# Kernel optimization log

Hardware: AMD Instinct MI355X
Metric: run time of the kernel (lower is better)

Reference implementation:

```python
import jax, jax.numpy as jnp
import numpy as np

B, S, HID, QK, H = 2, 2048, 2048, 2048, 16
DK, DV = QK // H, HID // H
EPS = 1e-5


def setup_inputs() -> dict:
    key = jax.random.key(0)
    ks = jax.random.split(key, 8)
    sd = 1.0 / np.sqrt(HID)
    inp = {
        "x": jax.random.normal(ks[0], (B, S, HID), jnp.float32),
        "wq": jax.random.normal(ks[1], (HID, QK), jnp.float32) * sd,
        "bq": jnp.zeros((QK,), jnp.float32),
        "wk": jax.random.normal(ks[2], (HID, QK), jnp.float32) * sd,
        "bk": jnp.zeros((QK,), jnp.float32),
        "wv": jax.random.normal(ks[3], (HID, HID), jnp.float32) * sd,
        "bv": jnp.zeros((HID,), jnp.float32),
        "wg": jax.random.normal(ks[4], (HID, HID), jnp.float32) * sd,
        "bg": jnp.zeros((HID,), jnp.float32),
        "wo": jax.random.normal(ks[5], (HID, HID), jnp.float32) * sd,
        "bo": jnp.zeros((HID,), jnp.float32),
        "gn_w": jnp.ones((HID,), jnp.float32),
        "gn_b": jnp.zeros((HID,), jnp.float32),
        # RetNet default gammas: 1 - exp(linspace(log(1/32), log(1/512), H))
        "gamma": 1.0 - jnp.exp(jnp.linspace(-np.log(32.0), -np.log(512.0), H)).astype(jnp.float32),
    }
    return inp


def reference(x, wq, bq, wk, bk, wv, bv, wg, bg, wo, bo, gn_w, gn_b, gamma):
    b, s, hid = x.shape
    h = gamma.shape[0]
    dk = wq.shape[1] // h
    dv = hid // h
    # projections + head split -> (b, h, s, d)
    q = (x @ wq + bq).reshape(b, s, h, dk).transpose(0, 2, 1, 3)
    k = (x @ wk + bk).reshape(b, s, h, dk).transpose(0, 2, 1, 3)
    v = (x @ wv + bv).reshape(b, s, h, dv).transpose(0, 2, 1, 3)
    # causal decay mask: gamma^(n-m) for n >= m else 0  -> (h, s, s)
    idx = jnp.arange(s)
    diff = idx[:, None] - idx[None, :]
    expn = jnp.maximum(diff, 0).astype(x.dtype)
    dmask = jnp.where(diff >= 0, gamma[:, None, None] ** expn, 0.0)
    # parallel retention
    scores = jnp.einsum('bhnd,bhmd->bhnm', q, k) * dmask
    ret = jnp.einsum('bhnm,bhmv->bhnv', scores, v)  # (b, h, s, dv)
    # GroupNorm(num_groups=h) over (b, hid, s): stats per (b, head) over (s, dv)
    mean = ret.mean(axis=(2, 3), keepdims=True)
    var = ((ret - mean) ** 2).mean(axis=(2, 3), keepdims=True)
    norm = (ret - mean) * jax.lax.rsqrt(var + EPS)
    norm = norm * gn_w.reshape(h, dv)[None, :, None, :] + gn_b.reshape(h, dv)[None, :, None, :]
    ro = norm.transpose(0, 2, 1, 3).reshape(b, s, hid)  # (b, s, hid)
    gate = jax.nn.silu(x @ wg + bg)
    out = (gate * ro) @ wo + bo
    return out
```

## Files before the change

kernel.cpp:

```cpp
#include <hip/hip_runtime.h>
#include <cstdint>
#include <cstddef>

#define DEVI __device__ __forceinline__

typedef unsigned short u16;
typedef __bf16 bf16_t;
typedef bf16_t bf16x8 __attribute__((ext_vector_type(8)));
typedef float f32x4 __attribute__((ext_vector_type(4)));

constexpr int BB = 2, SS = 2048, HID = 2048, NH = 16, DK = 128, DV = 128;
constexpr int MR = BB * SS;
constexpr int KD = HID;

DEVI u16 f2bf(float f) {
  union { float f; uint32_t u; } v; v.f = f;
  uint32_t u = v.u;
  uint32_t r = u + 0x7FFFu + ((u >> 16) & 1u);
  return (u16)(r >> 16);
}
DEVI float bf2f(u16 h) {
  union { uint32_t u; float f; } v; v.u = ((uint32_t)h) << 16;
  return v.f;
}
DEVI f32x4 mfma16(bf16x8 a, bf16x8 b, f32x4 c) {
  return __builtin_amdgcn_mfma_f32_16x16x32_bf16(a, b, c, 0, 0, 0);
}
DEVI void gload16(const u16* g, u16* l) {
  __builtin_amdgcn_global_load_lds(
      (const __attribute__((address_space(1))) uint32_t*)g,
      (__attribute__((address_space(3))) uint32_t*)l, 16, 0, 0);
}

__global__ __launch_bounds__(256) void castx_kernel(
    const float* __restrict__ x, u16* __restrict__ xb)
{
  size_t i = ((size_t)blockIdx.x * 256 + threadIdx.x) * 8;
  float4 a = *(const float4*)(x + i);
  float4 b = *(const float4*)(x + i + 4);
  ushort4 lo, hi;
  lo.x = f2bf(a.x); lo.y = f2bf(a.y); lo.z = f2bf(a.z); lo.w = f2bf(a.w);
  hi.x = f2bf(b.x); hi.y = f2bf(b.y); hi.z = f2bf(b.z); hi.w = f2bf(b.w);
  *(ushort4*)(xb + i) = lo;
  *(ushort4*)(xb + i + 4) = hi;
}

__global__ __launch_bounds__(256) void wtrans_kernel(
    const float* __restrict__ wq, const float* __restrict__ wk,
    const float* __restrict__ wv, const float* __restrict__ wg,
    const float* __restrict__ wo, u16* __restrict__ wt)
{
  __shared__ float t[32][33];
  const float* srcs[5] = {wq, wk, wv, wg, wo};
  const float* W = srcs[blockIdx.z];
  u16* dst = wt + (size_t)blockIdx.z * (size_t)KD * HID;
  int tx = threadIdx.x, ty = threadIdx.y;
  int c0 = blockIdx.x * 32, r0 = blockIdx.y * 32;
#pragma unroll
  for (int i = 0; i < 4; ++i)
    t[ty + i * 8][tx] = W[(size_t)(r0 + ty + i * 8) * HID + c0 + tx];
  __syncthreads();
#pragma unroll
  for (int i = 0; i < 4; ++i) {
    int n = c0 + ty + i * 8;
    int k = r0 + tx;
    dst[(size_t)n * KD + k] = f2bf(t[tx][ty + i * 8]);
  }
}

DEVI void gemm_core(const u16* __restrict__ A, const u16* __restrict__ Bt,
                    int m0, int n0, u16* sA, u16* sB, f32x4 (&acc)[4][4])
{
  const int tid = threadIdx.x;
  const int lane = tid & 63;
  const int wave = tid >> 6;
  const int wr = wave >> 1, wc = wave & 1;
  const int lhi = lane >> 4, llo = lane & 15;

  for (int kt = 0; kt < KD / 64; ++kt) {
    __syncthreads();
#pragma unroll
    for (int i = 0; i < 4; ++i) {
      int c = i * 256 + wave * 64 + lane;
      int row = c >> 3, scol = c & 7;
      int dcol = scol ^ (row & 7);
      gload16(A + (size_t)(m0 + row) * KD + kt * 64 + dcol * 8,
              sA + (i * 256 + wave * 64) * 8);
    }
#pragma unroll
    for (int i = 0; i < 4; ++i) {
      int c = i * 256 + wave * 64 + lane;
      int row = c >> 3, scol = c & 7;
      int dcol = scol ^ (row & 7);
      gload16(Bt + (size_t)(n0 + row) * KD + kt * 64 + dcol * 8,
              sB + (i * 256 + wave * 64) * 8);
    }
    __syncthreads();
#pragma unroll
    for (int ks = 0; ks < 2; ++ks) {
      const int kb = ks * 64 + lhi * 16;
      bf16x8 af[4], bfr[4];
#pragma unroll
      for (int mi = 0; mi < 4; ++mi) {
        int row = wr * 64 + mi * 16 + llo;
        af[mi] = *(const bf16x8*)((char*)sA + row * 128 + (kb ^ ((row & 7) << 4)));
      }
#pragma unroll
      for (int ni = 0; ni < 4; ++ni) {
        int row = wc * 64 + ni * 16 + llo;
        bfr[ni] = *(const bf16x8*)((char*)sB + row * 128 + (kb ^ ((row & 7) << 4)));
      }
#pragma unroll
      for (int mi = 0; mi < 4; ++mi)
#pragma unroll
        for (int ni = 0; ni < 4; ++ni)
          acc[mi][ni] = mfma16(af[mi], bfr[ni], acc[mi][ni]);
    }
  }
}

__global__ __launch_bounds__(256) void proj_kernel(
    const u16* __restrict__ xb, const u16* __restrict__ wtBase,
    const float* __restrict__ bq, const float* __restrict__ bk,
    const float* __restrict__ bv, const float* __restrict__ bg,
    u16* __restrict__ qb, u16* __restrict__ kb,
    u16* __restrict__ vtb, u16* __restrict__ gb)
{
  __shared__ u16 sA[128 * 64];
  __shared__ u16 sB[128 * 64];
  const int z = blockIdx.z;
  const u16* Bt = wtBase + (size_t)z * (size_t)KD * HID;
  f32x4 acc[4][4];
  const f32x4 zero = {0.f, 0.f, 0.f, 0.f};
#pragma unroll
  for (int mi = 0; mi < 4; ++mi)
#pragma unroll
    for (int ni = 0; ni < 4; ++ni) acc[mi][ni] = zero;

  const int m0 = blockIdx.x * 128, n0 = blockIdx.y * 128;
  gemm_core(xb, Bt, m0, n0, sA, sB, acc);

  const float* bias = (z == 0) ? bq : (z == 1) ? bk : (z == 2) ? bv : bg;
  const int lane = threadIdx.x & 63, wave = threadIdx.x >> 6;
  const int wr = wave >> 1, wc = wave & 1;
  const int lhi = lane >> 4, llo = lane & 15;
#pragma unroll
  for (int mi = 0; mi < 4; ++mi) {
#pragma unroll
    for (int ni = 0; ni < 4; ++ni) {
      int row0 = m0 + wr * 64 + mi * 16 + lhi * 4;
      int n = n0 + wc * 64 + ni * 16 + llo;
      float bsn = bias[n];
      if (z == 2) {
        int b = row0 >> 11, s0 = row0 & (SS - 1);
        int h = n >> 7, j = n & 127;
        ushort4 hv;
        hv.x = f2bf(acc[mi][ni][0] + bsn);
        hv.y = f2bf(acc[mi][ni][1] + bsn);
        hv.z = f2bf(acc[mi][ni][2] + bsn);
        hv.w = f2bf(acc[mi][ni][3] + bsn);
        *(ushort4*)(vtb + ((size_t)((b * NH + h) * DV + j)) * SS + s0) = hv;
      } else if (z == 3) {
#pragma unroll
        for (int r = 0; r < 4; ++r) {
          int m = row0 + r;
          float c = acc[mi][ni][r] + bsn;
          float sg = c / (1.0f + expf(-c));
          gb[(size_t)m * HID + n] = f2bf(sg);
        }
      } else {
        u16* dst = (z == 0) ? qb : kb;
#pragma unroll
        for (int r = 0; r < 4; ++r) {
          int m = row0 + r;
          int b = m >> 11, s = m & (SS - 1);
          int h = n >> 7, j = n & 127;
          dst[((size_t)((b * NH + h) * SS + s)) * DK + j] = f2bf(acc[mi][ni][r] + bsn);
        }
      }
    }
  }
}

__global__ __launch_bounds__(256) void retention_kernel(
    const u16* __restrict__ qb, const u16* __restrict__ kb,
    const u16* __restrict__ vtb, const float* __restrict__ gamma,
    float* __restrict__ ret, float* __restrict__ stats)
{
  __shared__ u16 sK[64 * 128];
  __shared__ u16 sV[128 * 64];
  __shared__ u16 sP[4][32 * 64];
  __shared__ float red[8];

  const int bh = blockIdx.y;
  const int n0 = blockIdx.x * 128;
  const int h = bh & (NH - 1);
  const float lg2 = log2f(gamma[h]);

  const int tid = threadIdx.x, lane = tid & 63, wave = tid >> 6;
  const int lhi = lane >> 4, llo = lane & 15;
  const int qrow = n0 + wave * 32;

  const u16* qbase = qb + ((size_t)bh * SS + qrow) * DK;
  bf16x8 aq[2][4];
#pragma unroll
  for (int mi = 0; mi < 2; ++mi)
#pragma unroll
    for (int ks = 0; ks < 4; ++ks)
      aq[mi][ks] = *(const bf16x8*)(qbase + (size_t)(mi * 16 + llo) * DK + ks * 32 + lhi * 8);

  float rdec[2][4];
#pragma unroll
  for (int mi = 0; mi < 2; ++mi)
#pragma unroll
    for (int r = 0; r < 4; ++r)
      rdec[mi][r] = exp2f(lg2 * (float)(qrow + mi * 16 + lhi * 4 + r));

  const f32x4 zero = {0.f, 0.f, 0.f, 0.f};
  f32x4 oacc[2][8];
#pragma unroll
  for (int mi = 0; mi < 2; ++mi)
#pragma unroll
    for (int nj = 0; nj < 8; ++nj) oacc[mi][nj] = zero;

  const u16* kbase = kb + (size_t)bh * SS * DK;
  const u16* vbase = vtb + (size_t)bh * DV * SS;
  const int mtiles = n0 / 64 + 2;

  for (int mt = 0; mt < mtiles; ++mt) {
    const int m0 = mt * 64;
    __syncthreads();
#pragma unroll
    for (int i = 0; i < 4; ++i) {
      int c = i * 256 + wave * 64 + lane;
      int row = c >> 4, scol = c & 15;
      int dcol = scol ^ (row & 15);
      gload16(kbase + (size_t)(m0 + row) * DK + dcol * 8,
              sK + (i * 256 + wave * 64) * 8);
    }
#pragma unroll
    for (int i = 0; i < 4; ++i) {
      int c = i * 256 + wave * 64 + lane;
      int row = c >> 3, scol = c & 7;
      int dcol = scol ^ (row & 7);
      gload16(vbase + (size_t)row * SS + m0 + dcol * 8,
              sV + (i * 256 + wave * 64) * 8);
    }
    __syncthreads();

    f32x4 sacc[2][4];
#pragma unroll
    for (int mi = 0; mi < 2; ++mi)
#pragma unroll
      for (int ni = 0; ni < 4; ++ni) sacc[mi][ni] = zero;
#pragma unroll
    for (int ks = 0; ks < 4; ++ks) {
      const int kbyte = ks * 64 + lhi * 16;
      bf16x8 bk_[4];
#pragma unroll
      for (int ni = 0; ni < 4; ++ni) {
        int row = ni * 16 + llo;
        bk_[ni] = *(const bf16x8*)((char*)sK + row * 256 + (kbyte ^ ((row & 15) << 4)));
      }
#pragma unroll
      for (int mi = 0; mi < 2; ++mi)
#pragma unroll
        for (int ni = 0; ni < 4; ++ni)
          sacc[mi][ni] = mfma16(aq[mi][ks], bk_[ni], sacc[mi][ni]);
    }

    float cfac[4];
#pragma unroll
    for (int ni = 0; ni < 4; ++ni)
      cfac[ni] = exp2f(-lg2 * (float)(m0 + ni * 16 + llo));
    const bool masked = (m0 + 63 > qrow);
    char* myP = (char*)&sP[wave][0];
#pragma unroll
    for (int mi = 0; mi < 2; ++mi) {
#pragma unroll
      for (int ni = 0; ni < 4; ++ni) {
#pragma unroll
        for (int r = 0; r < 4; ++r) {
          int prow = mi * 16 + lhi * 4 + r;
          int pcol = ni * 16 + llo;
          float w = rdec[mi][r] * cfac[ni];
          if (masked && (qrow + prow < m0 + pcol)) w = 0.0f;
          float p = sacc[mi][ni][r] * w;
          *(u16*)(myP + prow * 128 + ((pcol * 2) ^ ((prow & 7) << 4))) = f2bf(p);
        }
      }
    }

#pragma unroll
    for (int ks2 = 0; ks2 < 2; ++ks2) {
      const int kbyte = ks2 * 64 + lhi * 16;
      bf16x8 pa[2];
#pragma unroll
      for (int mi = 0; mi < 2; ++mi) {
        int row = mi * 16 + llo;
        pa[mi] = *(const bf16x8*)(myP + row * 128 + (kbyte ^ ((row & 7) << 4)));
      }
#pragma unroll
      for (int nj = 0; nj < 8; ++nj) {
        int row = nj * 16 + llo;
        bf16x8 vb = *(const bf16x8*)((char*)sV + row * 128 + (kbyte ^ ((row & 7) << 4)));
#pragma unroll
        for (int mi = 0; mi < 2; ++mi)
          oacc[mi][nj] = mfma16(pa[mi], vb, oacc[mi][nj]);
      }
    }
  }

  float lsum = 0.f, lsq = 0.f;
  float* rbase = ret + ((size_t)bh * SS + qrow) * DV;
#pragma unroll
  for (int mi = 0; mi < 2; ++mi) {
#pragma unroll
    for (int nj = 0; nj < 8; ++nj) {
      int prow0 = mi * 16 + lhi * 4;
      int j = nj * 16 + llo;
#pragma unroll
      for (int r = 0; r < 4; ++r) {
        float v = oacc[mi][nj][r];
        rbase[(size_t)(prow0 + r) * DV + j] = v;
        lsum += v; lsq += v * v;
      }
    }
  }
#pragma unroll
  for (int off = 32; off > 0; off >>= 1) {
    lsum += __shfl_down(lsum, off, 64);
    lsq  += __shfl_down(lsq,  off, 64);
  }
  if (lane == 0) { red[wave * 2] = lsum; red[wave * 2 + 1] = lsq; }
  __syncthreads();
  if (tid == 0) {
    float s = red[0] + red[2] + red[4] + red[6];
    float q = red[1] + red[3] + red[5] + red[7];
    atomicAdd(&stats[bh * 2], s);
    atomicAdd(&stats[bh * 2 + 1], q);
  }
}

__global__ __launch_bounds__(256) void normgate_kernel(
    const float* __restrict__ ret, const u16* __restrict__ gb,
    const float* __restrict__ stats, const float* __restrict__ gn_w,
    const float* __restrict__ gn_b, u16* __restrict__ a2)
{
  const int idx4 = (blockIdx.x * 256 + threadIdx.x) * 4;
  const int bh = idx4 >> 18;
  const int rem = idx4 & (SS * DV - 1);
  const int s = rem >> 7;
  const int dv = rem & (DV - 1);
  const float inv = 1.0f / (float)(SS * DV);
  float mean = stats[bh * 2] * inv;
  float var = stats[bh * 2 + 1] * inv - mean * mean;
  float rstd = rsqrtf(var + 1e-5f);
  const int b = bh >> 4, h = bh & (NH - 1);
  const int hd = h * DV + dv;
  float4 rv = *(const float4*)(ret + idx4);
  float4 w4 = *(const float4*)(gn_w + hd);
  float4 b4 = *(const float4*)(gn_b + hd);
  size_t gidx = ((size_t)(b * SS + s)) * HID + hd;
  ushort4 g4 = *(const ushort4*)(gb + gidx);
  ushort4 o;
  o.x = f2bf(bf2f(g4.x) * ((rv.x - mean) * rstd * w4.x + b4.x));
  o.y = f2bf(bf2f(g4.y) * ((rv.y - mean) * rstd * w4.y + b4.y));
  o.z = f2bf(bf2f(g4.z) * ((rv.z - mean) * rstd * w4.z + b4.z));
  o.w = f2bf(bf2f(g4.w) * ((rv.w - mean) * rstd * w4.w + b4.w));
  *(ushort4*)(a2 + gidx) = o;
}

__global__ __launch_bounds__(256) void final_kernel(
    const u16* __restrict__ a2, const u16* __restrict__ woT,
    const float* __restrict__ bo, float* __restrict__ out)
{
  __shared__ u16 sA[128 * 64];
  __shared__ u16 sB[128 * 64];
  f32x4 acc[4][4];
  const f32x4 zero = {0.f, 0.f, 0.f, 0.f};
#pragma unroll
  for (int mi = 0; mi < 4; ++mi)
#pragma unroll
    for (int ni = 0; ni < 4; ++ni) acc[mi][ni] = zero;

  const int m0 = blockIdx.x * 128, n0 = blockIdx.y * 128;
  gemm_core(a2, woT, m0, n0, sA, sB, acc);

  const int lane = threadIdx.x & 63, wave = threadIdx.x >> 6;
  const int wr = wave >> 1, wc = wave & 1;
  const int lhi = lane >> 4, llo = lane & 15;
#pragma unroll
  for (int mi = 0; mi < 4; ++mi) {
#pragma unroll
    for (int ni = 0; ni < 4; ++ni) {
      int row0 = m0 + wr * 64 + mi * 16 + lhi * 4;
      int n = n0 + wc * 64 + ni * 16 + llo;
      float bn = bo[n];
#pragma unroll
      for (int r = 0; r < 4; ++r)
        out[(size_t)(row0 + r) * HID + n] = acc[mi][ni][r] + bn;
    }
  }
}

extern "C" void kernel_launch(void* const* d_in, const int* in_sizes, int n_in,
                              void* d_out, int out_size, void* d_ws, size_t ws_size,
                              hipStream_t stream) {
  const float* x    = (const float*)d_in[0];
  const float* wq   = (const float*)d_in[1];
  const float* bq   = (const float*)d_in[2];
  const float* wk   = (const float*)d_in[3];
  const float* bk   = (const float*)d_in[4];
  const float* wv   = (const float*)d_in[5];
  const float* bv   = (const float*)d_in[6];
  const float* wg   = (const float*)d_in[7];
  const float* bg   = (const float*)d_in[8];
  const float* wo   = (const float*)d_in[9];
  const float* bo   = (const float*)d_in[10];
  const float* gn_w = (const float*)d_in[11];
  const float* gn_b = (const float*)d_in[12];
  const float* gam  = (const float*)d_in[13];

  char* ws = (char*)d_ws;
  u16* wT    = (u16*)(ws);
  u16* qb    = (u16*)(ws + 41943040);
  u16* kbuf  = (u16*)(ws + 58720256);
  u16* vtb   = (u16*)(ws + 75497472);
  u16* gb    = (u16*)(ws + 92274688);
  float* ret = (float*)(ws + 109051904);
  float* st  = (float*)(ws + 142606336);
  u16* a2    = qb;
  u16* xb    = (u16*)ret;

  hipMemsetAsync(st, 0, 256, stream);
  castx_kernel<<<4096, 256, 0, stream>>>(x, xb);
  wtrans_kernel<<<dim3(64, 64, 5), dim3(32, 8), 0, stream>>>(wq, wk, wv, wg, wo, wT);
  proj_kernel<<<dim3(32, 16, 4), 256, 0, stream>>>(xb, wT, bq, bk, bv, bg, qb, kbuf, vtb, gb);
  retention_kernel<<<dim3(16, 32), 256, 0, stream>>>(qb, kbuf, vtb, gam, ret, st);
  normgate_kernel<<<16384, 256, 0, stream>>>(ret, gb, st, gn_w, gn_b, a2);
  final_kernel<<<dim3(32, 16), 256, 0, stream>>>(a2, wT + (size_t)4 * KD * HID, bo, (float*)d_out);
}
```

Baseline: 555.7 us.

## Double-buffer GEMM and retention tiles, enlarge GEMM tiles, stage epilogue through LDS

The projection and output GEMMs move from 128x128 to 256x256 tiles with 512 threads and double-buffered LDS, so the load of the next K slice overlaps the MFMA work on the current one. The retention kernel also double-buffers its K/V tiles and raises wave priority around its MFMA sections. GEMM epilogues now go through swizzled LDS so global stores are coalesced 16-byte writes. Costs: 128KB of LDS per block and fewer blocks (128 for the final GEMM), which lowers occupancy and can leave CUs underused.

```diff
diff --git a/kernel.cpp b/kernel.cpp
--- a/kernel.cpp
+++ b/kernel.cpp
@@ -10,7 +10,6 @@
 typedef float f32x4 __attribute__((ext_vector_type(4)));
 
 constexpr int BB = 2, SS = 2048, HID = 2048, NH = 16, DK = 128, DV = 128;
-constexpr int MR = BB * SS;
 constexpr int KD = HID;
 
 DEVI u16 f2bf(float f) {
@@ -68,90 +67,100 @@
   }
 }
 
-DEVI void gemm_core(const u16* __restrict__ A, const u16* __restrict__ Bt,
-                    int m0, int n0, u16* sA, u16* sB, f32x4 (&acc)[4][4])
-{
-  const int tid = threadIdx.x;
-  const int lane = tid & 63;
-  const int wave = tid >> 6;
-  const int wr = wave >> 1, wc = wave & 1;
+DEVI void stage256(const u16* __restrict__ A, const u16* __restrict__ Bt,
+                   int m0, int n0, int kt, u16* sa, u16* sb, int tid)
+{
+#pragma unroll
+  for (int i = 0; i < 4; ++i) {
+    int c = i * 512 + tid;
+    int row = c >> 3, scol = c & 7, dcol = scol ^ (row & 7);
+    gload16(A + (size_t)(m0 + row) * KD + kt * 64 + dcol * 8, sa + c * 8);
+  }
+#pragma unroll
+  for (int i = 0; i < 4; ++i) {
+    int c = i * 512 + tid;
+    int row = c >> 3, scol = c & 7, dcol = scol ^ (row & 7);
+    gload16(Bt + (size_t)(n0 + row) * KD + kt * 64 + dcol * 8, sb + c * 8);
+  }
+}
+
+DEVI void gemm256(const u16* __restrict__ A, const u16* __restrict__ Bt,
+                  int m0, int n0, char* smem, f32x4 (&acc)[8][4])
+{
+  const int tid = threadIdx.x, lane = tid & 63, wave = tid >> 6;
+  const int wr = wave >> 2, wc = wave & 3;
   const int lhi = lane >> 4, llo = lane & 15;
 
+  stage256(A, Bt, m0, n0, 0, (u16*)smem, (u16*)(smem + 65536), tid);
+  asm volatile("s_waitcnt vmcnt(0)" ::: "memory");
+  __syncthreads();
+
   for (int kt = 0; kt < KD / 64; ++kt) {
-    __syncthreads();
-#pragma unroll
-    for (int i = 0; i < 4; ++i) {
-      int c = i * 256 + wave * 64 + lane;
-      int row = c >> 3, scol = c & 7;
-      int dcol = scol ^ (row & 7);
-      gload16(A + (size_t)(m0 + row) * KD + kt * 64 + dcol * 8,
-              sA + (i * 256 + wave * 64) * 8);
-    }
-#pragma unroll
-    for (int i = 0; i < 4; ++i) {
-      int c = i * 256 + wave * 64 + lane;
-      int row = c >> 3, scol = c & 7;
-      int dcol = scol ^ (row & 7);
-      gload16(Bt + (size_t)(n0 + row) * KD + kt * 64 + dcol * 8,
-              sB + (i * 256 + wave * 64) * 8);
-    }
-    __syncthreads();
+    char* cA = smem + (kt & 1) * 32768;
+    char* cB = smem + 65536 + (kt & 1) * 32768;
+    if (kt + 1 < KD / 64) {
+      u16* nA = (u16*)(smem + ((kt + 1) & 1) * 32768);
+      u16* nB = (u16*)(smem + 65536 + ((kt + 1) & 1) * 32768);
+      stage256(A, Bt, m0, n0, kt + 1, nA, nB, tid);
+    }
+    __builtin_amdgcn_s_setprio(1);
 #pragma unroll
     for (int ks = 0; ks < 2; ++ks) {
       const int kb = ks * 64 + lhi * 16;
-      bf16x8 af[4], bfr[4];
-#pragma unroll
-      for (int mi = 0; mi < 4; ++mi) {
-        int row = wr * 64 + mi * 16 + llo;
-        af[mi] = *(const bf16x8*)((char*)sA + row * 128 + (kb ^ ((row & 7) << 4)));
-      }
+      bf16x8 bfr[4];
 #pragma unroll
       for (int ni = 0; ni < 4; ++ni) {
         int row = wc * 64 + ni * 16 + llo;
-        bfr[ni] = *(const bf16x8*)((char*)sB + row * 128 + (kb ^ ((row & 7) << 4)));
-      }
-#pragma unroll
-      for (int mi = 0; mi < 4; ++mi)
+        bfr[ni] = *(const bf16x8*)(cB + row * 128 + (kb ^ ((row & 7) << 4)));
+      }
+#pragma unroll
+      for (int mi = 0; mi < 8; ++mi) {
+        int row = wr * 128 + mi * 16 + llo;
+        bf16x8 af = *(const bf16x8*)(cA + row * 128 + (kb ^ ((row & 7) << 4)));
 #pragma unroll
         for (int ni = 0; ni < 4; ++ni)
-          acc[mi][ni] = mfma16(af[mi], bfr[ni], acc[mi][ni]);
-    }
-  }
-}
-
-__global__ __launch_bounds__(256) void proj_kernel(
+          acc[mi][ni] = mfma16(af, bfr[ni], acc[mi][ni]);
+      }
+    }
+    __builtin_amdgcn_s_setprio(0);
+    asm volatile("s_waitcnt vmcnt(0)" ::: "memory");
+    __syncthreads();
+  }
+}
+
+__global__ __launch_bounds__(512, 2) void proj_kernel(
     const u16* __restrict__ xb, const u16* __restrict__ wtBase,
     const float* __restrict__ bq, const float* __restrict__ bk,
     const float* __restrict__ bv, const float* __restrict__ bg,
     u16* __restrict__ qb, u16* __restrict__ kb,
     u16* __restrict__ vtb, u16* __restrict__ gb)
 {
-  __shared__ u16 sA[128 * 64];
-  __shared__ u16 sB[128 * 64];
+  __shared__ __align__(16) char smem[131072];
   const int z = blockIdx.z;
   const u16* Bt = wtBase + (size_t)z * (size_t)KD * HID;
-  f32x4 acc[4][4];
+  f32x4 acc[8][4];
   const f32x4 zero = {0.f, 0.f, 0.f, 0.f};
 #pragma unroll
-  for (int mi = 0; mi < 4; ++mi)
+  for (int mi = 0; mi < 8; ++mi)
 #pragma unroll
     for (int ni = 0; ni < 4; ++ni) acc[mi][ni] = zero;
 
-  const int m0 = blockIdx.x * 128, n0 = blockIdx.y * 128;
-  gemm_core(xb, Bt, m0, n0, sA, sB, acc);
-
+  const int m0 = blockIdx.x * 256, n0 = blockIdx.y * 256;
+  gemm256(xb, Bt, m0, n0, smem, acc);
+
+  const int tid = threadIdx.x, lane = tid & 63, wave = tid >> 6;
+  const int wr = wave >> 2, wc = wave & 3;
+  const int lhi = lane >> 4, llo = lane & 15;
   const float* bias = (z == 0) ? bq : (z == 1) ? bk : (z == 2) ? bv : bg;
-  const int lane = threadIdx.x & 63, wave = threadIdx.x >> 6;
-  const int wr = wave >> 1, wc = wave & 1;
-  const int lhi = lane >> 4, llo = lane & 15;
-#pragma unroll
-  for (int mi = 0; mi < 4; ++mi) {
-#pragma unroll
-    for (int ni = 0; ni < 4; ++ni) {
-      int row0 = m0 + wr * 64 + mi * 16 + lhi * 4;
-      int n = n0 + wc * 64 + ni * 16 + llo;
-      float bsn = bias[n];
-      if (z == 2) {
+
+  if (z == 2) {
+#pragma unroll
+    for (int mi = 0; mi < 8; ++mi) {
+#pragma unroll
+      for (int ni = 0; ni < 4; ++ni) {
+        int row0 = m0 + wr * 128 + mi * 16 + lhi * 4;
+        int n = n0 + wc * 64 + ni * 16 + llo;
+        float bsn = bias[n];
         int b = row0 >> 11, s0 = row0 & (SS - 1);
         int h = n >> 7, j = n & 127;
         ushort4 hv;
@@ -160,23 +169,40 @@
         hv.z = f2bf(acc[mi][ni][2] + bsn);
         hv.w = f2bf(acc[mi][ni][3] + bsn);
         *(ushort4*)(vtb + ((size_t)((b * NH + h) * DV + j)) * SS + s0) = hv;
-      } else if (z == 3) {
+      }
+    }
+  } else {
+    u16* Lb = (u16*)smem;
+#pragma unroll
+    for (int mi = 0; mi < 8; ++mi) {
+#pragma unroll
+      for (int ni = 0; ni < 4; ++ni) {
+        int colL = wc * 64 + ni * 16 + llo;
+        float bsn = bias[n0 + colL];
 #pragma unroll
         for (int r = 0; r < 4; ++r) {
-          int m = row0 + r;
+          int rowL = wr * 128 + mi * 16 + lhi * 4 + r;
           float c = acc[mi][ni][r] + bsn;
-          float sg = c / (1.0f + expf(-c));
-          gb[(size_t)m * HID + n] = f2bf(sg);
+          if (z == 3) c = c / (1.0f + expf(-c));
+          Lb[rowL * 256 + (colL ^ (((rowL >> 2) & 3) << 4))] = f2bf(c);
         }
+      }
+    }
+    __syncthreads();
+    int rr = tid & 255, chh = tid >> 8;
+    int m = m0 + rr, b = m >> 11, s = m & (SS - 1);
+    int swz = ((rr >> 2) & 3) << 4;
+#pragma unroll
+    for (int jj = 0; jj < 16; ++jj) {
+      int c0 = chh * 128 + jj * 8;
+      uint4 v = *(const uint4*)&Lb[rr * 256 + (c0 ^ swz)];
+      int n = n0 + c0;
+      if (z == 3) {
+        *(uint4*)(gb + (size_t)m * HID + n) = v;
       } else {
+        int h = n >> 7, j2 = n & 127;
         u16* dst = (z == 0) ? qb : kb;
-#pragma unroll
-        for (int r = 0; r < 4; ++r) {
-          int m = row0 + r;
-          int b = m >> 11, s = m & (SS - 1);
-          int h = n >> 7, j = n & 127;
-          dst[((size_t)((b * NH + h) * SS + s)) * DK + j] = f2bf(acc[mi][ni][r] + bsn);
-        }
+        *(uint4*)(dst + ((size_t)((b * NH + h) * SS + s)) * DK + j2) = v;
       }
     }
   }
@@ -187,9 +213,7 @@
     const u16* __restrict__ vtb, const float* __restrict__ gamma,
     float* __restrict__ ret, float* __restrict__ stats)
 {
-  __shared__ u16 sK[64 * 128];
-  __shared__ u16 sV[128 * 64];
-  __shared__ u16 sP[4][32 * 64];
+  __shared__ __align__(16) char smemR[81920];
   __shared__ float red[8];
 
   const int bh = blockIdx.y;
@@ -227,32 +251,39 @@
   const u16* vbase = vtb + (size_t)bh * DV * SS;
   const int mtiles = n0 / 64 + 2;
 
+  auto stageKV = [&](int mbase, u16* sk, u16* sv) {
+#pragma unroll
+    for (int i = 0; i < 4; ++i) {
+      int c = i * 256 + tid;
+      int row = c >> 4, scol = c & 15, dcol = scol ^ (row & 15);
+      gload16(kbase + (size_t)(mbase + row) * DK + dcol * 8, sk + c * 8);
+    }
+#pragma unroll
+    for (int i = 0; i < 4; ++i) {
+      int c = i * 256 + tid;
+      int row = c >> 3, scol = c & 7, dcol = scol ^ (row & 7);
+      gload16(vbase + (size_t)row * SS + mbase + dcol * 8, sv + c * 8);
+    }
+  };
+
+  stageKV(0, (u16*)smemR, (u16*)(smemR + 32768));
+  asm volatile("s_waitcnt vmcnt(0)" ::: "memory");
+  __syncthreads();
+
   for (int mt = 0; mt < mtiles; ++mt) {
     const int m0 = mt * 64;
-    __syncthreads();
-#pragma unroll
-    for (int i = 0; i < 4; ++i) {
-      int c = i * 256 + wave * 64 + lane;
-      int row = c >> 4, scol = c & 15;
-      int dcol = scol ^ (row & 15);
-      gload16(kbase + (size_t)(m0 + row) * DK + dcol * 8,
-              sK + (i * 256 + wave * 64) * 8);
-    }
-#pragma unroll
-    for (int i = 0; i < 4; ++i) {
-      int c = i * 256 + wave * 64 + lane;
-      int row = c >> 3, scol = c & 7;
-      int dcol = scol ^ (row & 7);
-      gload16(vbase + (size_t)row * SS + m0 + dcol * 8,
-              sV + (i * 256 + wave * 64) * 8);
-    }
-    __syncthreads();
+    char* cK = smemR + (mt & 1) * 16384;
+    char* cV = smemR + 32768 + (mt & 1) * 16384;
+    if (mt + 1 < mtiles)
+      stageKV(m0 + 64, (u16*)(smemR + ((mt + 1) & 1) * 16384),
+              (u16*)(smemR + 32768 + ((mt + 1) & 1) * 16384));
 
     f32x4 sacc[2][4];
 #pragma unroll
     for (int mi = 0; mi < 2; ++mi)
 #pragma unroll
       for (int ni = 0; ni < 4; ++ni) sacc[mi][ni] = zero;
+    __builtin_amdgcn_s_setprio(1);
 #pragma unroll
     for (int ks = 0; ks < 4; ++ks) {
       const int kbyte = ks * 64 + lhi * 16;
@@ -260,7 +291,7 @@
 #pragma unroll
       for (int ni = 0; ni < 4; ++ni) {
         int row = ni * 16 + llo;
-        bk_[ni] = *(const bf16x8*)((char*)sK + row * 256 + (kbyte ^ ((row & 15) << 4)));
+        bk_[ni] = *(const bf16x8*)(cK + row * 256 + (kbyte ^ ((row & 15) << 4)));
       }
 #pragma unroll
       for (int mi = 0; mi < 2; ++mi)
@@ -268,13 +299,14 @@
         for (int ni = 0; ni < 4; ++ni)
           sacc[mi][ni] = mfma16(aq[mi][ks], bk_[ni], sacc[mi][ni]);
     }
+    __builtin_amdgcn_s_setprio(0);
 
     float cfac[4];
 #pragma unroll
     for (int ni = 0; ni < 4; ++ni)
       cfac[ni] = exp2f(-lg2 * (float)(m0 + ni * 16 + llo));
     const bool masked = (m0 + 63 > qrow);
-    char* myP = (char*)&sP[wave][0];
+    char* myP = smemR + 65536 + wave * 4096;
 #pragma unroll
     for (int mi = 0; mi < 2; ++mi) {
 #pragma unroll
@@ -291,6 +323,7 @@
       }
     }
 
+    __builtin_amdgcn_s_setprio(1);
 #pragma unroll
     for (int ks2 = 0; ks2 < 2; ++ks2) {
       const int kbyte = ks2 * 64 + lhi * 16;
@@ -303,12 +336,15 @@
 #pragma unroll
       for (int nj = 0; nj < 8; ++nj) {
         int row = nj * 16 + llo;
-        bf16x8 vb = *(const bf16x8*)((char*)sV + row * 128 + (kbyte ^ ((row & 7) << 4)));
+        bf16x8 vb = *(const bf16x8*)(cV + row * 128 + (kbyte ^ ((row & 7) << 4)));
 #pragma unroll
         for (int mi = 0; mi < 2; ++mi)
           oacc[mi][nj] = mfma16(pa[mi], vb, oacc[mi][nj]);
       }
     }
+    __builtin_amdgcn_s_setprio(0);
+    asm volatile("s_waitcnt vmcnt(0)" ::: "memory");
+    __syncthreads();
   }
 
   float lsum = 0.f, lsq = 0.f;
@@ -371,36 +407,55 @@
   *(ushort4*)(a2 + gidx) = o;
 }
 
-__global__ __launch_bounds__(256) void final_kernel(
+__global__ __launch_bounds__(512, 2) void final_kernel(
     const u16* __restrict__ a2, const u16* __restrict__ woT,
     const float* __restrict__ bo, float* __restrict__ out)
 {
-  __shared__ u16 sA[128 * 64];
-  __shared__ u16 sB[128 * 64];
-  f32x4 acc[4][4];
+  __shared__ __align__(16) char smem[131072];
+  f32x4 acc[8][4];
   const f32x4 zero = {0.f, 0.f, 0.f, 0.f};
 #pragma unroll
-  for (int mi = 0; mi < 4; ++mi)
+  for (int mi = 0; mi < 8; ++mi)
 #pragma unroll
     for (int ni = 0; ni < 4; ++ni) acc[mi][ni] = zero;
 
-  const int m0 = blockIdx.x * 128, n0 = blockIdx.y * 128;
-  gemm_core(a2, woT, m0, n0, sA, sB, acc);
-
-  const int lane = threadIdx.x & 63, wave = threadIdx.x >> 6;
-  const int wr = wave >> 1, wc = wave & 1;
+  const int m0 = blockIdx.x * 256, n0 = blockIdx.y * 256;
+  gemm256(a2, woT, m0, n0, smem, acc);
+
+  const int tid = threadIdx.x, lane = tid & 63, wave = tid >> 6;
+  const int wr = wave >> 2, wc = wave & 3;
   const int lhi = lane >> 4, llo = lane & 15;
-#pragma unroll
-  for (int mi = 0; mi < 4; ++mi) {
-#pragma unroll
-    for (int ni = 0; ni < 4; ++ni) {
-      int row0 = m0 + wr * 64 + mi * 16 + lhi * 4;
-      int n = n0 + wc * 64 + ni * 16 + llo;
-      float bn = bo[n];
-#pragma unroll
-      for (int r = 0; r < 4; ++r)
-        out[(size_t)(row0 + r) * HID + n] = acc[mi][ni][r] + bn;
-    }
+  float* Lf = (float*)smem;
+
+#pragma unroll
+  for (int pass = 0; pass < 2; ++pass) {
+    if ((wc >> 1) == pass) {
+#pragma unroll
+      for (int mi = 0; mi < 8; ++mi) {
+#pragma unroll
+        for (int ni = 0; ni < 4; ++ni) {
+          int colL = (wc & 1) * 64 + ni * 16 + llo;
+          float bn = bo[n0 + pass * 128 + colL];
+#pragma unroll
+          for (int r = 0; r < 4; ++r) {
+            int rowL = wr * 128 + mi * 16 + lhi * 4 + r;
+            Lf[rowL * 128 + (colL ^ (((rowL >> 2) & 1) << 4))] =
+                acc[mi][ni][r] + bn;
+          }
+        }
+      }
+    }
+    __syncthreads();
+    int rr = tid & 255, chh = tid >> 8;
+    int m = m0 + rr;
+    int swz = ((rr >> 2) & 1) << 4;
+#pragma unroll
+    for (int jj = 0; jj < 16; ++jj) {
+      int c0 = chh * 64 + jj * 4;
+      float4 v = *(const float4*)&Lf[rr * 128 + (c0 ^ swz)];
+      *(float4*)(out + (size_t)m * HID + n0 + pass * 128 + c0) = v;
+    }
+    __syncthreads();
   }
 }
 
@@ -436,8 +491,8 @@
   hipMemsetAsync(st, 0, 256, stream);
   castx_kernel<<<4096, 256, 0, stream>>>(x, xb);
   wtrans_kernel<<<dim3(64, 64, 5), dim3(32, 8), 0, stream>>>(wq, wk, wv, wg, wo, wT);
-  proj_kernel<<<dim3(32, 16, 4), 256, 0, stream>>>(xb, wT, bq, bk, bv, bg, qb, kbuf, vtb, gb);
+  proj_kernel<<<dim3(16, 8, 4), 512, 0, stream>>>(xb, wT, bq, bk, bv, bg, qb, kbuf, vtb, gb);
   retention_kernel<<<dim3(16, 32), 256, 0, stream>>>(qb, kbuf, vtb, gam, ret, st);
   normgate_kernel<<<16384, 256, 0, stream>>>(ret, gb, st, gn_w, gn_b, a2);
-  final_kernel<<<dim3(32, 16), 256, 0, stream>>>(a2, wT + (size_t)4 * KD * HID, bo, (float*)d_out);
-}
+  final_kernel<<<dim3(16, 8), 512, 0, stream>>>(a2, wT + (size_t)4 * KD * HID, bo, (float*)d_out);
+}
```

Result: no change. 552.9 us (-0.5%).
